# Kernel optimization log

Measured on AMD Instinct MI355X. Metric: run time of the kernel, lower is better.

The kernel has to match this reference:

```python
import jax, jax.numpy as jnp
import numpy as np

S, L, D = 50, 1024, 768
D4 = D // 4

def _ln(x, g, b, eps=1e-5):
    m = jnp.mean(x, axis=-1, keepdims=True)
    v = jnp.mean((x - m) ** 2, axis=-1, keepdims=True)
    return (x - m) * jax.lax.rsqrt(v + eps) * g + b

def _attn(x, Wq, Wk, Wv):
    # x: [N, D]; low-rank q/k (D4), values are the raw input, then output proj Wv.
    q = x @ Wq                      # [N, D4]
    k = x @ Wk                      # [N, D4]
    u = (q @ k.T) / jnp.sqrt(jnp.float32(q.shape[-1]))
    a = jax.nn.softmax(u, axis=-1)  # [N, N]
    return (a @ x) @ Wv             # [N, D]

def setup_inputs() -> dict:
    key = jax.random.key(0)
    ks = jax.random.split(key, 16)
    g = lambda i, shape: jax.random.normal(ks[i], shape, dtype=jnp.float32) * 0.02
    return dict(
        x=jax.random.normal(ks[0], (S, L, D), dtype=jnp.float32),
        pre_Wq=g(1, (S, D, D4)), pre_Wk=g(2, (S, D, D4)), pre_Wv=g(3, (S, D, D)),
        ln1_g=jnp.ones((S, D)), ln1_b=jnp.zeros((S, D)),
        pre_W1=g(4, (S, D, D4)), pre_b1=jnp.zeros((S, D4)),
        pre_W2=g(5, (S, D4, D)), pre_b2=jnp.zeros((S, D)),
        ln4p_g=jnp.ones((S, D)), ln4p_b=jnp.zeros((S, D)),
        cross_Wq=g(6, (D, D4)), cross_Wk=g(7, (D, D4)), cross_Wv=g(8, (D, D)),
        ln2_g=jnp.ones((D,)), ln2_b=jnp.zeros((D,)),
        post_Wq=g(9, (S, D, D4)), post_Wk=g(10, (S, D, D4)), post_Wv=g(11, (S, D, D)),
        ln3_g=jnp.ones((S, D)), ln3_b=jnp.zeros((S, D)),
        post_W1=g(12, (S, D, D4)), post_b1=jnp.zeros((S, D4)),
        post_W2=g(13, (S, D4, D)), post_b2=jnp.zeros((S, D)),
        ln4_g=jnp.ones((S, D)), ln4_b=jnp.zeros((S, D)),
    )

def reference(x, pre_Wq, pre_Wk, pre_Wv, ln1_g, ln1_b,
              pre_W1, pre_b1, pre_W2, pre_b2, ln4p_g, ln4p_b,
              cross_Wq, cross_Wk, cross_Wv, ln2_g, ln2_b,
              post_Wq, post_Wk, post_Wv, ln3_g, ln3_b,
              post_W1, post_b1, post_W2, post_b2, ln4_g, ln4_b):
    # step_wise forward; dropout is identity at inference.
    # pre_self_step: per-step Attention (step dim vmapped == loop over n_step)
    h = jax.vmap(_attn)(x, pre_Wq, pre_Wk, pre_Wv)          # [S, L, D]
    x = jax.vmap(_ln)(x + h, ln1_g, ln1_b)
    # pre_mlp: per-step bottleneck MLP
    h = jax.nn.relu(jnp.einsum('sld,sdf->slf', x, pre_W1) + pre_b1[:, None, :])
    h = jnp.einsum('slf,sfd->sld', h, pre_W2) + pre_b2[:, None, :]
    x = jax.vmap(_ln)(x + h, ln4p_g, ln4p_b)
    # cross_step: shared Attention over the step axis (seq positions as batch)
    xt = jnp.transpose(x, (1, 0, 2))                        # [L, S, D]
    h = jax.vmap(_attn, in_axes=(0, None, None, None))(xt, cross_Wq, cross_Wk, cross_Wv)
    xt = _ln(xt + h, ln2_g, ln2_b)
    x = jnp.transpose(xt, (1, 0, 2))                        # [S, L, D]
    # post_self_step
    h = jax.vmap(_attn)(x, post_Wq, post_Wk, post_Wv)
    x = jax.vmap(_ln)(x + h, ln3_g, ln3_b)
    # post_mlp
    h = jax.nn.relu(jnp.einsum('sld,sdf->slf', x, post_W1) + post_b1[:, None, :])
    h = jnp.einsum('slf,sfd->sld', h, post_W2) + post_b2[:, None, :]
    x = jax.vmap(_ln)(x + h, ln4_g, ln4_b)
    return x
```

## Files before the change

### kernel.cpp

```cpp
#include <hip/hip_runtime.h>


typedef __bf16 bf16x8 __attribute__((ext_vector_type(8)));
typedef __bf16 bf16x4 __attribute__((ext_vector_type(4)));
typedef float f32x4 __attribute__((ext_vector_type(4)));

typedef __attribute__((address_space(3))) void lds_t;
typedef __attribute__((address_space(1))) const void gbl_t;

__device__ __forceinline__ void gload16(const void* g, void* l) {
    __builtin_amdgcn_global_load_lds((gbl_t*)g, (lds_t*)l, 16, 0, 0);
}

__global__ __launch_bounds__(256) void gemm128_k(
    const __bf16* __restrict__ A, const __bf16* __restrict__ Bt, __bf16* __restrict__ C,
    int M, int N, int K, int lda, int ldb, int ldc,
    long long sA, long long sB, long long sC,
    const float* __restrict__ bias, long long sBias, int relu)
{
    __shared__ __bf16 As[128 * 64];
    __shared__ __bf16 Bs[128 * 64];

    const int batch = blockIdx.z;
    A  += (long long)batch * sA;
    Bt += (long long)batch * sB;
    C  += (long long)batch * sC;

    const int m0 = blockIdx.x * 128;
    const int n0 = blockIdx.y * 128;
    const int tid  = threadIdx.x;
    const int lane = tid & 63;
    const int wave = tid >> 6;
    const int wr = wave >> 1, wc = wave & 1;
    const int l15 = lane & 15;

    const __bf16* aSrc[4];
    const __bf16* bSrc[4];
    #pragma unroll
    for (int r = 0; r < 4; r++) {
        const int g   = r * 256 + tid;
        const int row = g >> 3;
        const int ch  = (g & 7) ^ (row & 7);
        int ra = m0 + row; if (ra > M - 1) ra = M - 1;
        int rb = n0 + row; if (rb > N - 1) rb = N - 1;
        aSrc[r] = A  + (long long)ra * lda + (ch << 3);
        bSrc[r] = Bt + (long long)rb * ldb + (ch << 3);
    }
    __bf16* aD = As + wave * 512;
    __bf16* bD = Bs + wave * 512;

    f32x4 acc[4][4];
    #pragma unroll
    for (int i = 0; i < 4; i++)
        #pragma unroll
        for (int j = 0; j < 4; j++) acc[i][j] = f32x4{0.f, 0.f, 0.f, 0.f};

    for (int kb = 0; kb < K; kb += 64) {
        #pragma unroll
        for (int r = 0; r < 4; r++) gload16(aSrc[r] + kb, aD + r * 2048);
        #pragma unroll
        for (int r = 0; r < 4; r++) gload16(bSrc[r] + kb, bD + r * 2048);
        __syncthreads();

        #pragma unroll
        for (int ks = 0; ks < 2; ks++) {
            const int cg = ks * 4 + (lane >> 4);
            const int so = ((cg ^ (l15 & 7)) << 3);
            bf16x8 av[4], bv[4];
            #pragma unroll
            for (int mi = 0; mi < 4; mi++)
                av[mi] = *(const bf16x8*)&As[(wr * 64 + mi * 16 + l15) * 64 + so];
            #pragma unroll
            for (int ni = 0; ni < 4; ni++)
                bv[ni] = *(const bf16x8*)&Bs[(wc * 64 + ni * 16 + l15) * 64 + so];
            #pragma unroll
            for (int mi = 0; mi < 4; mi++)
                #pragma unroll
                for (int ni = 0; ni < 4; ni++)
                    acc[mi][ni] = __builtin_amdgcn_mfma_f32_16x16x32_bf16(
                        av[mi], bv[ni], acc[mi][ni], 0, 0, 0);
        }
        __syncthreads();
    }

    const int rb4 = (lane >> 4) << 2;
    #pragma unroll
    for (int mi = 0; mi < 4; mi++) {
        #pragma unroll
        for (int ni = 0; ni < 4; ni++) {
            const int col = n0 + wc * 64 + ni * 16 + l15;
            if (col >= N) continue;
            float bvl = 0.f;
            if (bias) bvl = bias[(long long)batch * sBias + col];
            #pragma unroll
            for (int r = 0; r < 4; r++) {
                const int row = m0 + wr * 64 + mi * 16 + rb4 + r;
                if (row < M) {
                    float v = acc[mi][ni][r] + bvl;
                    if (relu) v = fmaxf(v, 0.f);
                    C[(long long)row * ldc + col] = (__bf16)v;
                }
            }
        }
    }
}

template<int INF32>
__global__ __launch_bounds__(256) void trans_k(
    const void* __restrict__ in, __bf16* __restrict__ out,
    int R, int Cn, long long sIn, long long sOut)
{
    __shared__ float tile[32][33];
    const int b  = blockIdx.z;
    const int r0 = blockIdx.x * 32, c0 = blockIdx.y * 32;
    const int t  = threadIdx.x;
    {
        const int rl = t >> 3;
        const int cl = (t & 7) << 2;
        const long long src = (long long)b * sIn + (long long)(r0 + rl) * Cn + c0 + cl;
        if (INF32) {
            float4 v = *(const float4*)((const float*)in + src);
            tile[rl][cl + 0] = v.x; tile[rl][cl + 1] = v.y;
            tile[rl][cl + 2] = v.z; tile[rl][cl + 3] = v.w;
        } else {
            bf16x4 v = *(const bf16x4*)((const __bf16*)in + src);
            tile[rl][cl + 0] = (float)v[0]; tile[rl][cl + 1] = (float)v[1];
            tile[rl][cl + 2] = (float)v[2]; tile[rl][cl + 3] = (float)v[3];
        }
    }
    __syncthreads();
    {
        const int c2 = t >> 3;
        const int r2 = (t & 7) << 2;
        bf16x4 o;
        o[0] = (__bf16)tile[r2 + 0][c2]; o[1] = (__bf16)tile[r2 + 1][c2];
        o[2] = (__bf16)tile[r2 + 2][c2]; o[3] = (__bf16)tile[r2 + 3][c2];
        *(bf16x4*)(out + (long long)b * sOut + (long long)(c0 + c2) * R + r0 + r2) = o;
    }
}

template<int BNN, int BF32>
__global__ __launch_bounds__(256) void gemm_k(
    const __bf16* __restrict__ A, const void* __restrict__ Bv, __bf16* __restrict__ C,
    int M, int N, int K, int Kb,
    int lda, int ldb, int ldc,
    long long sA, long long sB, long long sC,
    const float* __restrict__ bias, long long sBias, int relu)
{
    __shared__ __bf16 As[64][72];
    __shared__ __bf16 Bs[64][72];

    const int batch = blockIdx.z;
    A += (long long)batch * sA;
    C += (long long)batch * sC;

    const int m0 = blockIdx.x * 64;
    const int n0 = blockIdx.y * 64;
    const int tid = threadIdx.x;
    const int lane = tid & 63;
    const int wave = tid >> 6;
    const int wr = wave >> 1, wc = wave & 1;

    f32x4 acc[2][2];
    #pragma unroll
    for (int i = 0; i < 2; i++)
        #pragma unroll
        for (int j = 0; j < 2; j++) acc[i][j] = f32x4{0.f, 0.f, 0.f, 0.f};

    for (int kb = 0; kb < K; kb += 64) {
        {
            const int row = tid >> 2;
            const int cs = (tid & 3) << 4;
            const int gr = m0 + row;
            __bf16* dst = &As[row][cs];
            if (gr < M) {
                const __bf16* src = A + (long long)gr * lda + kb + cs;
                *(bf16x8*)dst       = *(const bf16x8*)src;
                *(bf16x8*)(dst + 8) = *(const bf16x8*)(src + 8);
            } else {
                #pragma unroll
                for (int i = 0; i < 16; i++) dst[i] = (__bf16)0.f;
            }
        }
        if (BNN) {
            const int kk = tid >> 2;
            const int ns = (tid & 3) << 4;
            const int gk = kb + kk;
            const bool kok = gk < Kb;
            const __bf16* src = (const __bf16*)Bv + (long long)batch * sB
                              + (long long)gk * ldb + n0 + ns;
            if (kok && (n0 + ns + 16 <= N)) {
                bf16x8 v0 = *(const bf16x8*)src;
                bf16x8 v1 = *(const bf16x8*)(src + 8);
                #pragma unroll
                for (int i = 0; i < 8; i++) Bs[ns + i][kk] = v0[i];
                #pragma unroll
                for (int i = 0; i < 8; i++) Bs[ns + 8 + i][kk] = v1[i];
            } else {
                for (int i = 0; i < 16; i++) {
                    const int n = n0 + ns + i;
                    Bs[ns + i][kk] = (kok && n < N) ? src[i] : (__bf16)0.f;
                }
            }
        } else {
            const int row = tid >> 2;
            const int cs = (tid & 3) << 4;
            const int gn = n0 + row;
            __bf16* dst = &Bs[row][cs];
            if (gn < N) {
                const __bf16* src = (const __bf16*)Bv + (long long)batch * sB
                                  + (long long)gn * ldb + kb + cs;
                *(bf16x8*)dst       = *(const bf16x8*)src;
                *(bf16x8*)(dst + 8) = *(const bf16x8*)(src + 8);
            } else {
                #pragma unroll
                for (int i = 0; i < 16; i++) dst[i] = (__bf16)0.f;
            }
        }
        __syncthreads();

        #pragma unroll
        for (int ks = 0; ks < 64; ks += 32) {
            const int kf = ks + ((lane >> 4) << 3);
            bf16x8 av[2], bv[2];
            #pragma unroll
            for (int mi = 0; mi < 2; mi++)
                av[mi] = *(const bf16x8*)&As[wr * 32 + mi * 16 + (lane & 15)][kf];
            #pragma unroll
            for (int ni = 0; ni < 2; ni++)
                bv[ni] = *(const bf16x8*)&Bs[wc * 32 + ni * 16 + (lane & 15)][kf];
            #pragma unroll
            for (int mi = 0; mi < 2; mi++)
                #pragma unroll
                for (int ni = 0; ni < 2; ni++)
                    acc[mi][ni] = __builtin_amdgcn_mfma_f32_16x16x32_bf16(
                        av[mi], bv[ni], acc[mi][ni], 0, 0, 0);
        }
        __syncthreads();
    }

    const int rb = (lane >> 4) << 2;
    const int cc = lane & 15;
    #pragma unroll
    for (int mi = 0; mi < 2; mi++) {
        #pragma unroll
        for (int ni = 0; ni < 2; ni++) {
            const int col = n0 + wc * 32 + ni * 16 + cc;
            if (col >= N) continue;
            float bvl = 0.f;
            if (bias) bvl = bias[(long long)batch * sBias + col];
            #pragma unroll
            for (int r = 0; r < 4; r++) {
                const int row = m0 + wr * 32 + mi * 16 + rb + r;
                if (row < M) {
                    float v = acc[mi][ni][r] + bvl;
                    if (relu) v = fmaxf(v, 0.f);
                    C[(long long)row * ldc + col] = (__bf16)v;
                }
            }
        }
    }
}

__device__ __forceinline__ float wave_sum(float v) {
    #pragma unroll
    for (int o = 32; o > 0; o >>= 1) v += __shfl_xor(v, o);
    return v;
}
__device__ __forceinline__ float wave_max(float v) {
    #pragma unroll
    for (int o = 32; o > 0; o >>= 1) v = fmaxf(v, __shfl_xor(v, o));
    return v;
}

__global__ __launch_bounds__(256) void softmax_self_k(__bf16* __restrict__ u, float scale) {
    __shared__ float red[4];
    const long long row = blockIdx.x;
    __bf16* p = u + row * 1024;
    const int t = threadIdx.x;
    bf16x4 raw = *(const bf16x4*)(p + t * 4);
    float v[4];
    float mx = -1e30f;
    #pragma unroll
    for (int i = 0; i < 4; i++) { v[i] = (float)raw[i]; mx = fmaxf(mx, v[i]); }
    mx = wave_max(mx);
    if ((t & 63) == 0) red[t >> 6] = mx;
    __syncthreads();
    mx = fmaxf(fmaxf(red[0], red[1]), fmaxf(red[2], red[3]));
    float s = 0.f;
    #pragma unroll
    for (int i = 0; i < 4; i++) { v[i] = __expf(scale * (v[i] - mx)); s += v[i]; }
    s = wave_sum(s);
    __syncthreads();
    if ((t & 63) == 0) red[t >> 6] = s;
    __syncthreads();
    s = red[0] + red[1] + red[2] + red[3];
    const float inv = 1.f / s;
    bf16x4 o;
    #pragma unroll
    for (int i = 0; i < 4; i++) o[i] = (__bf16)(v[i] * inv);
    *(bf16x4*)(p + t * 4) = o;
}

__global__ __launch_bounds__(256) void softmax_cross_k(__bf16* __restrict__ u, float scale) {
    const long long row = (long long)blockIdx.x * 4 + (threadIdx.x >> 6);
    __bf16* p = u + row * 64;
    const int lane = threadIdx.x & 63;
    float v = (lane < 50) ? (float)p[lane] : -1e30f;
    float mx = wave_max(v);
    float e = (lane < 50) ? __expf(scale * (v - mx)) : 0.f;
    float s = wave_sum(e);
    p[lane] = (__bf16)(e / s);
}

__global__ __launch_bounds__(192) void add_ln_k(
    const __bf16* __restrict__ x, const __bf16* __restrict__ h, void* __restrict__ out,
    const float* __restrict__ g, const float* __restrict__ b, int mode, int outf32)
{
    __shared__ float red[3];
    const long long r = blockIdx.x;
    const __bf16* xr = x + r * 768;
    const __bf16* hr = h + r * 768;
    long long orow; const float *gp, *bp;
    if (mode == 0) {
        orow = r;
        const long long s = r >> 10;
        gp = g + s * 768; bp = b + s * 768;
    } else {
        const long long l = r / 50, s2 = r % 50;
        orow = s2 * 1024 + l;
        gp = g; bp = b;
    }
    const int t = threadIdx.x;
    const int d = t * 4;
    bf16x4 xv = *(const bf16x4*)(xr + d);
    bf16x4 hv = *(const bf16x4*)(hr + d);
    float v[4]; float sum = 0.f;
    #pragma unroll
    for (int i = 0; i < 4; i++) { v[i] = (float)xv[i] + (float)hv[i]; sum += v[i]; }
    sum = wave_sum(sum);
    if ((t & 63) == 0) red[t >> 6] = sum;
    __syncthreads();
    const float mean = (red[0] + red[1] + red[2]) * (1.f / 768.f);
    float vs = 0.f;
    #pragma unroll
    for (int i = 0; i < 4; i++) { const float dd = v[i] - mean; vs += dd * dd; }
    vs = wave_sum(vs);
    __syncthreads();
    if ((t & 63) == 0) red[t >> 6] = vs;
    __syncthreads();
    const float rstd = rsqrtf((red[0] + red[1] + red[2]) * (1.f / 768.f) + 1e-5f);
    float4 gv = *(const float4*)(gp + d);
    float4 bv = *(const float4*)(bp + d);
    const float o0 = (v[0] - mean) * rstd * gv.x + bv.x;
    const float o1 = (v[1] - mean) * rstd * gv.y + bv.y;
    const float o2 = (v[2] - mean) * rstd * gv.z + bv.z;
    const float o3 = (v[3] - mean) * rstd * gv.w + bv.w;
    if (outf32) {
        float4 o{o0, o1, o2, o3};
        *(float4*)((float*)out + orow * 768 + d) = o;
    } else {
        bf16x4 o;
        o[0] = (__bf16)o0; o[1] = (__bf16)o1; o[2] = (__bf16)o2; o[3] = (__bf16)o3;
        *(bf16x4*)((__bf16*)out + orow * 768 + d) = o;
    }
}

__global__ __launch_bounds__(192) void transpose_sl_k(const __bf16* __restrict__ in,
                                                      __bf16* __restrict__ out) {
    const long long r = (long long)blockIdx.x * 2 + (threadIdx.x >= 96);
    const int c = (threadIdx.x % 96) * 8;
    const long long s = r >> 10, l = r & 1023;
    *(bf16x8*)(out + (l * 50 + s) * 768 + c) = *(const bf16x8*)(in + r * 768 + c);
}

__global__ __launch_bounds__(256) void cvt_f32_bf16_k(const float* __restrict__ in,
                                                      __bf16* __restrict__ out) {
    const long long i = ((long long)blockIdx.x * 256 + threadIdx.x) * 8;
    float4 a = *(const float4*)(in + i);
    float4 b = *(const float4*)(in + i + 4);
    bf16x8 o;
    o[0] = (__bf16)a.x; o[1] = (__bf16)a.y; o[2] = (__bf16)a.z; o[3] = (__bf16)a.w;
    o[4] = (__bf16)b.x; o[5] = (__bf16)b.y; o[6] = (__bf16)b.z; o[7] = (__bf16)b.w;
    *(bf16x8*)(out + i) = o;
}

extern "C" void kernel_launch(void* const* d_in, const int* in_sizes, int n_in,
                              void* d_out, int out_size, void* d_ws, size_t ws_size,
                              hipStream_t stream)
{
    const float SCALE = 0.07216878364870322f;
    auto inf = [&](int i) { return (const float*)d_in[i]; };

    char* w = (char*)d_ws;
    __bf16* xw = (__bf16*)(w + 0LL);
    __bf16* hw = (__bf16*)(w + 78643200LL);
    __bf16* tw = (__bf16*)(w + 157286400LL);
    __bf16* xt = (__bf16*)(w + 235929600LL);
    __bf16* qw = (__bf16*)(w + 314572800LL);
    __bf16* kw = (__bf16*)(w + 334233600LL);
    __bf16* G  = (__bf16*)(w + 353894400LL);
    __bf16* wa = G;
    if (ws_size < 458752000ULL) return;

    auto g128 = [&](const __bf16* A, const __bf16* Bt, __bf16* C,
                    int M, int N, int K, int lda, int ldb, int ldc,
                    long long sA, long long sB, long long sC, int batch,
                    const float* bias, long long sBias, int relu) {
        dim3 grid((M + 127) / 128, (N + 127) / 128, batch);
        gemm128_k<<<grid, dim3(256), 0, stream>>>(A, Bt, C, M, N, K, lda, ldb, ldc,
                                                  sA, sB, sC, bias, sBias, relu);
    };
    auto transw = [&](const float* W, __bf16* outp, int R, int Cn, int batch) {
        dim3 grid(R / 32, Cn / 32, batch);
        trans_k<1><<<grid, dim3(256), 0, stream>>>(W, outp, R, Cn,
                                                   (long long)R * Cn, (long long)R * Cn);
    };

    cvt_f32_bf16_k<<<19200, 256, 0, stream>>>(inf(0), xw);

    auto self_attn = [&](const float* Wq, const float* Wk, const float* Wv,
                         const float* g, const float* b) {
        transw(Wq, wa, 768, 192, 50);
        g128(xw, wa, qw, 1024, 192, 768, 768, 768, 192,
             786432LL, 147456LL, 196608LL, 50, nullptr, 0, 0);
        transw(Wk, wa, 768, 192, 50);
        g128(xw, wa, kw, 1024, 192, 768, 768, 768, 192,
             786432LL, 147456LL, 196608LL, 50, nullptr, 0, 0);
        g128(qw, kw, G, 1024, 1024, 192, 192, 192, 1024,
             196608LL, 196608LL, 1048576LL, 50, nullptr, 0, 0);
        softmax_self_k<<<51200, 256, 0, stream>>>(G, SCALE);
        {
            dim3 grid(32, 24, 50);
            trans_k<0><<<grid, dim3(256), 0, stream>>>(xw, hw, 1024, 768,
                                                       786432LL, 786432LL);
        }
        g128(G, hw, tw, 1024, 768, 1024, 1024, 1024, 768,
             1048576LL, 786432LL, 786432LL, 50, nullptr, 0, 0);
        transw(Wv, wa, 768, 768, 50);
        g128(tw, wa, hw, 1024, 768, 768, 768, 768, 768,
             786432LL, 589824LL, 786432LL, 50, nullptr, 0, 0);
        add_ln_k<<<51200, 192, 0, stream>>>(xw, hw, xw, g, b, 0, 0);
    };
    auto mlp = [&](const float* W1, const float* b1, const float* W2, const float* b2,
                   const float* g, const float* b, void* outp, int outf32) {
        transw(W1, wa, 768, 192, 50);
        g128(xw, wa, qw, 1024, 192, 768, 768, 768, 192,
             786432LL, 147456LL, 196608LL, 50, b1, 192LL, 1);
        transw(W2, wa, 192, 768, 50);
        g128(qw, wa, hw, 1024, 768, 192, 192, 192, 768,
             196608LL, 147456LL, 786432LL, 50, b2, 768LL, 0);
        add_ln_k<<<51200, 192, 0, stream>>>(xw, hw, outp, g, b, 0, outf32);
    };

    self_attn(inf(1), inf(2), inf(3), inf(4), inf(5));
    mlp(inf(6), inf(7), inf(8), inf(9), inf(10), inf(11), xw, 0);

    transpose_sl_k<<<25600, 192, 0, stream>>>(xw, xt);
    transw(inf(12), wa, 768, 192, 1);
    g128(xt, wa, qw, 51200, 192, 768, 768, 768, 192, 0, 0, 0, 1, nullptr, 0, 0);
    transw(inf(13), wa, 768, 192, 1);
    g128(xt, wa, kw, 51200, 192, 768, 768, 768, 192, 0, 0, 0, 1, nullptr, 0, 0);
    {
        dim3 grid(1, 1, 1024);
        gemm_k<0, 0><<<grid, dim3(256), 0, stream>>>(qw, kw, G, 50, 50, 192, 192,
                                                     192, 192, 64, 9600LL, 9600LL,
                                                     3200LL, nullptr, 0, 0);
    }
    softmax_cross_k<<<12800, 256, 0, stream>>>(G, SCALE);
    {
        dim3 grid(1, 12, 1024);
        gemm_k<1, 0><<<grid, dim3(256), 0, stream>>>(G, xt, tw, 50, 768, 64, 50,
                                                     64, 768, 768, 3200LL, 38400LL,
                                                     38400LL, nullptr, 0, 0);
    }
    transw(inf(14), qw, 768, 768, 1);
    g128(tw, qw, hw, 51200, 768, 768, 768, 768, 768, 0, 0, 0, 1, nullptr, 0, 0);
    add_ln_k<<<51200, 192, 0, stream>>>(xt, hw, xw, inf(15), inf(16), 1, 0);

    self_attn(inf(17), inf(18), inf(19), inf(20), inf(21));
    mlp(inf(22), inf(23), inf(24), inf(25), inf(26), inf(27), d_out, 1);
}
```

Before: 2.548 ms.

## Double-buffer GEMM LDS tiles and fuse Q/K projections into one GEMM

The 128x128 GEMM now uses two LDS buffers and issues global-to-LDS loads for the next K tile before computing the current one, overlapping memory latency with MFMA work. The Q and K projections are merged into a single GEMM with N=384 over concatenated transposed weights, so the input activations are read once instead of twice and one launch is removed. The doubled LDS footprint may reduce occupancy.

```diff
diff --git a/kernel.cpp b/kernel.cpp
--- a/kernel.cpp
+++ b/kernel.cpp
@@ -18,8 +18,8 @@
     long long sA, long long sB, long long sC,
     const float* __restrict__ bias, long long sBias, int relu)
 {
-    __shared__ __bf16 As[128 * 64];
-    __shared__ __bf16 Bs[128 * 64];
+    __shared__ __bf16 As[2][128 * 64];
+    __shared__ __bf16 Bs[2][128 * 64];
 
     const int batch = blockIdx.z;
     A  += (long long)batch * sA;
@@ -46,8 +46,7 @@
         aSrc[r] = A  + (long long)ra * lda + (ch << 3);
         bSrc[r] = Bt + (long long)rb * ldb + (ch << 3);
     }
-    __bf16* aD = As + wave * 512;
-    __bf16* bD = Bs + wave * 512;
+    const int ldsOff = wave * 512;
 
     f32x4 acc[4][4];
     #pragma unroll
@@ -55,13 +54,24 @@
         #pragma unroll
         for (int j = 0; j < 4; j++) acc[i][j] = f32x4{0.f, 0.f, 0.f, 0.f};
 
-    for (int kb = 0; kb < K; kb += 64) {
-        #pragma unroll
-        for (int r = 0; r < 4; r++) gload16(aSrc[r] + kb, aD + r * 2048);
-        #pragma unroll
-        for (int r = 0; r < 4; r++) gload16(bSrc[r] + kb, bD + r * 2048);
-        __syncthreads();
-
+    const int nt = K >> 6;
+    #pragma unroll
+    for (int r = 0; r < 4; r++) gload16(aSrc[r], &As[0][ldsOff + r * 2048]);
+    #pragma unroll
+    for (int r = 0; r < 4; r++) gload16(bSrc[r], &Bs[0][ldsOff + r * 2048]);
+    __syncthreads();
+
+    for (int t = 0; t < nt; ++t) {
+        const int buf = t & 1;
+        if (t + 1 < nt) {
+            const int kb = (t + 1) << 6;
+            #pragma unroll
+            for (int r = 0; r < 4; r++)
+                gload16(aSrc[r] + kb, &As[buf ^ 1][ldsOff + r * 2048]);
+            #pragma unroll
+            for (int r = 0; r < 4; r++)
+                gload16(bSrc[r] + kb, &Bs[buf ^ 1][ldsOff + r * 2048]);
+        }
         #pragma unroll
         for (int ks = 0; ks < 2; ks++) {
             const int cg = ks * 4 + (lane >> 4);
@@ -69,10 +79,10 @@
             bf16x8 av[4], bv[4];
             #pragma unroll
             for (int mi = 0; mi < 4; mi++)
-                av[mi] = *(const bf16x8*)&As[(wr * 64 + mi * 16 + l15) * 64 + so];
+                av[mi] = *(const bf16x8*)&As[buf][(wr * 64 + mi * 16 + l15) * 64 + so];
             #pragma unroll
             for (int ni = 0; ni < 4; ni++)
-                bv[ni] = *(const bf16x8*)&Bs[(wc * 64 + ni * 16 + l15) * 64 + so];
+                bv[ni] = *(const bf16x8*)&Bs[buf][(wc * 64 + ni * 16 + l15) * 64 + so];
             #pragma unroll
             for (int mi = 0; mi < 4; mi++)
                 #pragma unroll
@@ -398,7 +408,6 @@
     __bf16* tw = (__bf16*)(w + 157286400LL);
     __bf16* xt = (__bf16*)(w + 235929600LL);
     __bf16* qw = (__bf16*)(w + 314572800LL);
-    __bf16* kw = (__bf16*)(w + 334233600LL);
     __bf16* G  = (__bf16*)(w + 353894400LL);
     __bf16* wa = G;
     if (ws_size < 458752000ULL) return;
@@ -411,24 +420,23 @@
         gemm128_k<<<grid, dim3(256), 0, stream>>>(A, Bt, C, M, N, K, lda, ldb, ldc,
                                                   sA, sB, sC, bias, sBias, relu);
     };
-    auto transw = [&](const float* W, __bf16* outp, int R, int Cn, int batch) {
+    auto transw = [&](const float* W, __bf16* outp, int R, int Cn, int batch,
+                      long long sOut) {
         dim3 grid(R / 32, Cn / 32, batch);
         trans_k<1><<<grid, dim3(256), 0, stream>>>(W, outp, R, Cn,
-                                                   (long long)R * Cn, (long long)R * Cn);
+                                                   (long long)R * Cn, sOut);
     };
 
     cvt_f32_bf16_k<<<19200, 256, 0, stream>>>(inf(0), xw);
 
     auto self_attn = [&](const float* Wq, const float* Wk, const float* Wv,
                          const float* g, const float* b) {
-        transw(Wq, wa, 768, 192, 50);
-        g128(xw, wa, qw, 1024, 192, 768, 768, 768, 192,
-             786432LL, 147456LL, 196608LL, 50, nullptr, 0, 0);
-        transw(Wk, wa, 768, 192, 50);
-        g128(xw, wa, kw, 1024, 192, 768, 768, 768, 192,
-             786432LL, 147456LL, 196608LL, 50, nullptr, 0, 0);
-        g128(qw, kw, G, 1024, 1024, 192, 192, 192, 1024,
-             196608LL, 196608LL, 1048576LL, 50, nullptr, 0, 0);
+        transw(Wq, wa,          768, 192, 50, 294912LL);
+        transw(Wk, wa + 147456, 768, 192, 50, 294912LL);
+        g128(xw, wa, qw, 1024, 384, 768, 768, 768, 384,
+             786432LL, 294912LL, 393216LL, 50, nullptr, 0, 0);
+        g128(qw, qw + 192, G, 1024, 1024, 192, 384, 384, 1024,
+             393216LL, 393216LL, 1048576LL, 50, nullptr, 0, 0);
         softmax_self_k<<<51200, 256, 0, stream>>>(G, SCALE);
         {
             dim3 grid(32, 24, 50);
@@ -437,17 +445,17 @@
         }
         g128(G, hw, tw, 1024, 768, 1024, 1024, 1024, 768,
              1048576LL, 786432LL, 786432LL, 50, nullptr, 0, 0);
-        transw(Wv, wa, 768, 768, 50);
+        transw(Wv, wa, 768, 768, 50, 589824LL);
         g128(tw, wa, hw, 1024, 768, 768, 768, 768, 768,
              786432LL, 589824LL, 786432LL, 50, nullptr, 0, 0);
         add_ln_k<<<51200, 192, 0, stream>>>(xw, hw, xw, g, b, 0, 0);
     };
     auto mlp = [&](const float* W1, const float* b1, const float* W2, const float* b2,
                    const float* g, const float* b, void* outp, int outf32) {
-        transw(W1, wa, 768, 192, 50);
+        transw(W1, wa, 768, 192, 50, 147456LL);
         g128(xw, wa, qw, 1024, 192, 768, 768, 768, 192,
              786432LL, 147456LL, 196608LL, 50, b1, 192LL, 1);
-        transw(W2, wa, 192, 768, 50);
+        transw(W2, wa, 192, 768, 50, 147456LL);
         g128(qw, wa, hw, 1024, 768, 192, 192, 192, 768,
              196608LL, 147456LL, 786432LL, 50, b2, 768LL, 0);
         add_ln_k<<<51200, 192, 0, stream>>>(xw, hw, outp, g, b, 0, outf32);
@@ -457,14 +465,13 @@
     mlp(inf(6), inf(7), inf(8), inf(9), inf(10), inf(11), xw, 0);
 
     transpose_sl_k<<<25600, 192, 0, stream>>>(xw, xt);
-    transw(inf(12), wa, 768, 192, 1);
-    g128(xt, wa, qw, 51200, 192, 768, 768, 768, 192, 0, 0, 0, 1, nullptr, 0, 0);
-    transw(inf(13), wa, 768, 192, 1);
-    g128(xt, wa, kw, 51200, 192, 768, 768, 768, 192, 0, 0, 0, 1, nullptr, 0, 0);
+    transw(inf(12), wa,          768, 192, 1, 0);
+    transw(inf(13), wa + 147456, 768, 192, 1, 0);
+    g128(xt, wa, qw, 51200, 384, 768, 768, 768, 384, 0, 0, 0, 1, nullptr, 0, 0);
     {
         dim3 grid(1, 1, 1024);
-        gemm_k<0, 0><<<grid, dim3(256), 0, stream>>>(qw, kw, G, 50, 50, 192, 192,
-                                                     192, 192, 64, 9600LL, 9600LL,
+        gemm_k<0, 0><<<grid, dim3(256), 0, stream>>>(qw, qw + 192, G, 50, 50, 192, 192,
+                                                     384, 384, 64, 19200LL, 19200LL,
                                                      3200LL, nullptr, 0, 0);
     }
     softmax_cross_k<<<12800, 256, 0, stream>>>(G, SCALE);
@@ -474,7 +481,7 @@
                                                      64, 768, 768, 3200LL, 38400LL,
                                                      38400LL, nullptr, 0, 0);
     }
-    transw(inf(14), qw, 768, 768, 1);
+    transw(inf(14), qw, 768, 768, 1, 0);
     g128(tw, qw, hw, 51200, 768, 768, 768, 768, 768, 0, 0, 0, 1, nullptr, 0, 0);
     add_ln_k<<<51200, 192, 0, stream>>>(xt, hw, xw, inf(15), inf(16), 1, 0);
 
```

Result: no change. 2.581 ms (+1.3%).
